# Optimization experiments

Hardware: AMD Instinct MI355X
Metric: run time of the kernel (lower is better)

## Reference

```python
import jax, jax.numpy as jnp
import numpy as np

D_MODEL = 2048
NUM_HEADS = 16
HEAD_DIM = D_MODEL // NUM_HEADS
SCALE = HEAD_DIM ** -0.5
ALPHA = 1.0


def setup_inputs() -> dict:
    key = jax.random.key(0)
    ks = jax.random.split(key, 9)
    B, T = 2, 2048
    s = 0.02
    w = lambda k: jax.random.normal(k, (D_MODEL, D_MODEL), jnp.float32) * s
    b = lambda k: jax.random.normal(k, (D_MODEL,), jnp.float32) * s
    return {
        'x': jax.random.normal(ks[0], (B, T, D_MODEL), jnp.float32),
        'q_w': w(ks[1]), 'q_b': b(ks[2]),
        'k_w': w(ks[3]), 'k_b': b(ks[4]),
        'v_w': w(ks[5]), 'v_b': b(ks[6]),
        'o_w': w(ks[7]), 'o_b': b(ks[8]),
    }


def reference(x, q_w, q_b, k_w, k_b, v_w, v_b, o_w, o_b):
    B, T, D = x.shape
    H, HD = NUM_HEADS, HEAD_DIM

    def proj_split(w, bias):
        y = x @ w.T + bias  # torch Linear: x @ W^T + b
        # B T (H D) -> (B H) T D
        return y.reshape(B, T, H, HD).transpose(0, 2, 1, 3).reshape(B * H, T, HD)

    Q = proj_split(q_w, q_b)
    K = proj_split(k_w, k_b)
    V = proj_split(v_w, v_b)

    # Note: original computes S[h,i,j] = K_i . Q_j (K first, Q second)
    S = jnp.einsum('hid,hjd->hij', K, Q) * SCALE  # (B*H, T, T)

    idx = jnp.arange(T)
    delta = idx[:, None] - idx[None, :]  # delta[i,j] = i - j
    # similarity_power_law decay: -(delta**alpha) for delta>=0, else 0
    decay = jnp.where(delta < 0, 0.0, -(delta.astype(jnp.float32) ** ALPHA))
    # causal mask: positions with j > i (delta < 0) set to -inf, then add decay
    S = jnp.where(delta < 0, -jnp.inf, S) + decay

    C = jax.nn.softmax(S, axis=-1)
    attn = jnp.einsum('hij,hjd->hid', C, V)  # (B*H, T, HD)
    # (B H) T D -> B T (H D)
    attn = attn.reshape(B, H, T, HD).transpose(0, 2, 1, 3).reshape(B, T, D)
    return attn @ o_w.T + o_b
```

## Files before the change

### kernel.cpp

```cpp
#include <hip/hip_runtime.h>
#include <hip/hip_bf16.h>
#include <stdint.h>

#define BT    4096
#define DM    2048
#define TSEQ  2048
#define NHEAD 16
#define HD    128
#define QKV_LD 6144
#define ATT_SCALE 0.088388347648318447f
#define WIN   64

typedef __attribute__((ext_vector_type(8))) short short8;
typedef __attribute__((ext_vector_type(4))) float f32x4;

__device__ __forceinline__ uint16_t f2bf(float f) {
  uint32_t u = __float_as_uint(f);
  return (uint16_t)((u + 0x7FFFu + ((u >> 16) & 1u)) >> 16);
}

__device__ __forceinline__ void gload_lds16(const void* g, void* l) {
  __builtin_amdgcn_global_load_lds((__attribute__((address_space(1))) void*)g,
                                   (__attribute__((address_space(3))) void*)l,
                                   16, 0, 0);
}

__global__ __launch_bounds__(256) void prep(const float* __restrict__ x,
                                            const float* __restrict__ qw,
                                            const float* __restrict__ kw,
                                            const float* __restrict__ vw,
                                            const float* __restrict__ ow,
                                            const float* __restrict__ qb,
                                            const float* __restrict__ kb,
                                            const float* __restrict__ vb,
                                            uint16_t* __restrict__ xb,
                                            uint16_t* __restrict__ wqkv,
                                            uint16_t* __restrict__ wo,
                                            float* __restrict__ bcat) {
  const int NX = BT * DM / 4;
  const int NW = DM * DM / 4;
  const int total = NX + 4 * NW;
  int i0 = blockIdx.x * 256 + threadIdx.x;
  for (int idx = i0; idx < total; idx += gridDim.x * 256) {
    const float* src;
    uint16_t* dst;
    int off;
    if (idx < NX)            { src = x;  dst = xb;                          off = idx; }
    else if (idx < NX + NW)  { src = qw; dst = wqkv;                        off = idx - NX; }
    else if (idx < NX + 2*NW){ src = kw; dst = wqkv + (size_t)DM * DM;      off = idx - NX - NW; }
    else if (idx < NX + 3*NW){ src = vw; dst = wqkv + (size_t)2 * DM * DM;  off = idx - NX - 2*NW; }
    else                     { src = ow; dst = wo;                          off = idx - NX - 3*NW; }
    float4 v = ((const float4*)src)[off];
    ushort4 o;
    o.x = f2bf(v.x); o.y = f2bf(v.y); o.z = f2bf(v.z); o.w = f2bf(v.w);
    ((ushort4*)dst)[off] = o;
  }
  if (i0 < 3 * DM) {
    float v = (i0 < DM) ? qb[i0] : (i0 < 2 * DM ? kb[i0 - DM] : vb[i0 - 2 * DM]);
    bcat[i0] = v;
  }
}

template <int MF, bool OUT_BF16>
__global__ __launch_bounds__(512, 1) void gemm_p4(const uint16_t* __restrict__ A,
                                                  const uint16_t* __restrict__ B,
                                                  const float* __restrict__ bias,
                                                  void* __restrict__ Cout,
                                                  int M, int N, int K) {
  constexpr int BM   = MF * 32;
  constexpr int ABUF = BM * 32;
  constexpr int BUFE = ABUF + 8192;
  constexpr int MB   = (MF == 8) ? 2 : 4;
  constexpr int NB   = 8 / MB;
  __shared__ uint16_t sm[4 * BUFE];

  const int tid = threadIdx.x;
  const int l   = tid & 63;
  const int wid = tid >> 6;
  const int wr  = wid >> 2;
  const int wc  = wid & 3;
  const int ln  = l & 15;
  const int g   = l >> 4;

  const int nbx    = N >> 8;
  const int bid    = blockIdx.x;
  const int xcd    = bid & 7;
  const int idx    = bid >> 3;
  const int rect_n = nbx / NB;
  const int rect_m = (M / BM) / MB;
  const int m_t    = (xcd / NB) * rect_m + idx / rect_n;
  const int n_t    = (xcd % NB) * rect_n + idx % rect_n;
  const int m0     = m_t * BM;
  const int n0     = n_t << 8;

  const int srow = l >> 2;
  const int gch  = (l & 3) ^ ((l >> 3) & 3);
  const uint16_t* pa  = A + (size_t)(m0 + wid * 16 + srow) * K + gch * 8;
  const uint16_t* pb0 = B + (size_t)(n0 + wid * 16 + srow) * K + gch * 8;
  const uint16_t* pb1 = B + (size_t)(n0 + 128 + wid * 16 + srow) * K + gch * 8;
  const int ldsA  = wid * 512;
  const int ldsB0 = ABUF + wid * 512;
  const int ldsB1 = ABUF + 4096 + wid * 512;

  const int pc = g ^ ((ln >> 1) & 3);

  f32x4 acc[MF][4];
#pragma unroll
  for (int i = 0; i < MF; ++i)
#pragma unroll
    for (int j = 0; j < 4; ++j) acc[i][j] = (f32x4){0.f, 0.f, 0.f, 0.f};

  const int nt = K >> 5;

#define STAGE(T)                                                        \
  {                                                                     \
    uint16_t* base_ = sm + (size_t)((T) & 3) * BUFE;                    \
    const size_t ko_ = (size_t)(T) * 32;                                \
    gload_lds16(pa + ko_, base_ + ldsA);                                \
    if (MF == 8) gload_lds16(pa + (size_t)128 * K + ko_, base_ + 4096 + ldsA); \
    gload_lds16(pb0 + ko_, base_ + ldsB0);                              \
    gload_lds16(pb1 + ko_, base_ + ldsB1);                              \
  }

#define COMPUTE(T)                                                      \
  {                                                                     \
    const uint16_t* buf_ = sm + (size_t)((T) & 3) * BUFE;               \
    short8 af_[MF], bf_[4];                                             \
    _Pragma("unroll")                                                   \
    for (int fi = 0; fi < MF; ++fi)                                     \
      af_[fi] = *(const short8*)(buf_ + (wr * (MF * 16) + fi * 16 + ln) * 32 + pc * 8); \
    _Pragma("unroll")                                                   \
    for (int fj = 0; fj < 4; ++fj)                                      \
      bf_[fj] = *(const short8*)(buf_ + ABUF + (wc * 64 + fj * 16 + ln) * 32 + pc * 8); \
    __builtin_amdgcn_s_setprio(1);                                      \
    _Pragma("unroll")                                                   \
    for (int fi = 0; fi < MF; ++fi)                                     \
      _Pragma("unroll")                                                 \
      for (int fj = 0; fj < 4; ++fj)                                    \
        acc[fi][fj] = __builtin_amdgcn_mfma_f32_16x16x32_bf16(          \
            af_[fi], bf_[fj], acc[fi][fj], 0, 0, 0);                    \
    __builtin_amdgcn_s_setprio(0);                                      \
  }

#define WAIT_LOOP()                                                     \
  if (MF == 8) asm volatile("s_waitcnt vmcnt(8)" ::: "memory");         \
  else         asm volatile("s_waitcnt vmcnt(6)" ::: "memory");
#define WAIT_PEEL1()                                                    \
  if (MF == 8) asm volatile("s_waitcnt vmcnt(4)" ::: "memory");         \
  else         asm volatile("s_waitcnt vmcnt(3)" ::: "memory");

  STAGE(0); STAGE(1); STAGE(2);
  WAIT_LOOP();
  __builtin_amdgcn_s_barrier();

#pragma unroll 1
  for (int t = 0; t < nt - 3; ++t) {
    STAGE(t + 3);
    COMPUTE(t);
    WAIT_LOOP();
    __builtin_amdgcn_s_barrier();
  }
  COMPUTE(nt - 3);
  WAIT_PEEL1();
  __builtin_amdgcn_s_barrier();
  COMPUTE(nt - 2);
  asm volatile("s_waitcnt vmcnt(0)" ::: "memory");
  __builtin_amdgcn_s_barrier();
  COMPUTE(nt - 1);
#undef STAGE
#undef COMPUTE
#undef WAIT_LOOP
#undef WAIT_PEEL1

  const int g4 = g * 4;
#pragma unroll
  for (int fi = 0; fi < MF; ++fi) {
    size_t row = (size_t)(m0 + wr * (MF * 16) + fi * 16 + g4);
#pragma unroll
    for (int fj = 0; fj < 4; ++fj) {
      int col = n0 + wc * 64 + fj * 16 + ln;
      float bv = bias[col];
#pragma unroll
      for (int r = 0; r < 4; ++r) {
        float v = acc[fi][fj][r] + bv;
        if (OUT_BF16) ((uint16_t*)Cout)[(row + r) * N + col] = f2bf(v);
        else          ((float*)Cout)[(row + r) * N + col] = v;
      }
    }
  }
}

__global__ __launch_bounds__(256) void attn_mfma(const uint16_t* __restrict__ QKV,
                                                 uint16_t* __restrict__ O) {
  __shared__ __align__(16) uint16_t smem[16384 + 17408];
  uint16_t* Qs = smem;
  uint16_t* Vt = smem + 16384;
  uint16_t* Pl = smem;

  const int tid  = threadIdx.x;
  const int lane = tid & 63;
  const int w    = tid >> 6;
  const int g    = lane >> 4;
  const int ln   = lane & 15;

  const int i0 = blockIdx.x * 64;
  const int h  = blockIdx.y;
  const int b  = blockIdx.z;
  const int wb = i0 - 63;
  const size_t hoff  = (size_t)h * HD;
  const size_t bbase = (size_t)b * TSEQ;

#pragma unroll
  for (int it = 0; it < 8; ++it) {
    int s   = it * 256 + tid;
    int row = s >> 4, c = s & 15;
    int j = wb + row;
    if (j >= 0 && j < TSEQ) {
      const uint16_t* gsrc = QKV + (bbase + j) * (size_t)QKV_LD + hoff
                           + (size_t)((c ^ (row & 7)) * 8);
      uint16_t* ldst = Qs + (size_t)(s & ~63) * 8;
      gload_lds16(gsrc, ldst);
    } else {
      uint4 z = {0, 0, 0, 0};
      *(uint4*)(Qs + (size_t)s * 8) = z;
    }
  }

#pragma unroll
  for (int it = 0; it < 4; ++it) {
    int s  = it * 256 + tid;
    int jp = (s & 15) | (it << 4);
    int dc = (s >> 4) & 15;
    int j0 = wb + 2 * jp;
    uint4 va = {0, 0, 0, 0}, vb = {0, 0, 0, 0};
    if (j0 >= 0 && j0 < TSEQ)
      va = *(const uint4*)(QKV + (bbase + j0) * (size_t)QKV_LD + 2 * DM + hoff + dc * 8);
    if (j0 + 1 >= 0 && j0 + 1 < TSEQ)
      vb = *(const uint4*)(QKV + (bbase + j0 + 1) * (size_t)QKV_LD + 2 * DM + hoff + dc * 8);
    const uint16_t* ap = (const uint16_t*)&va;
    const uint16_t* bp = (const uint16_t*)&vb;
#pragma unroll
    for (int t = 0; t < 8; ++t) {
      uint32_t pk = (uint32_t)ap[t] | ((uint32_t)bp[t] << 16);
      *(uint32_t*)(Vt + (size_t)(dc * 8 + t) * 136 + 2 * jp) = pk;
    }
  }

  short8 kreg[4];
  {
    const uint16_t* kp = QKV + (bbase + i0 + w * 16 + ln) * (size_t)QKV_LD
                       + DM + hoff + g * 8;
#pragma unroll
    for (int kc = 0; kc < 4; ++kc) kreg[kc] = *(const short8*)(kp + kc * 32);
  }

  __syncthreads();

  f32x4 acc[8];
#pragma unroll
  for (int nf = 0; nf < 8; ++nf) acc[nf] = (f32x4){0.f, 0.f, 0.f, 0.f};
#pragma unroll
  for (int kc = 0; kc < 4; ++kc) {
#pragma unroll
    for (int nf = 0; nf < 8; ++nf) {
      int row = nf * 16 + ln;
      int chunk = (kc * 4 + g) ^ (row & 7);
      short8 qf = *(const short8*)(Qs + (size_t)row * 128 + chunk * 8);
      acc[nf] = __builtin_amdgcn_mfma_f32_16x16x32_bf16(kreg[kc], qf, acc[nf], 0, 0, 0);
    }
  }

#pragma unroll
  for (int nf = 0; nf < 8; ++nf) {
    int rj = nf * 16 + ln;
    int jg = wb + rj;
#pragma unroll
    for (int r = 0; r < 4; ++r) {
      int il = w * 16 + g * 4 + r;
      int delta = il + 63 - rj;
      float v = acc[nf][r] * ATT_SCALE - (float)delta;
      acc[nf][r] = ((unsigned)delta < 64u && jg >= 0) ? v : -1e30f;
    }
  }

  float inv[4];
#pragma unroll
  for (int r = 0; r < 4; ++r) {
    float mx = acc[0][r];
#pragma unroll
    for (int nf = 1; nf < 8; ++nf) mx = fmaxf(mx, acc[nf][r]);
    mx = fmaxf(mx, __shfl_xor(mx, 1));
    mx = fmaxf(mx, __shfl_xor(mx, 2));
    mx = fmaxf(mx, __shfl_xor(mx, 4));
    mx = fmaxf(mx, __shfl_xor(mx, 8));
    float s = 0.f;
#pragma unroll
    for (int nf = 0; nf < 8; ++nf) {
      float e = __expf(acc[nf][r] - mx);
      acc[nf][r] = e;
      s += e;
    }
    s += __shfl_xor(s, 1);
    s += __shfl_xor(s, 2);
    s += __shfl_xor(s, 4);
    s += __shfl_xor(s, 8);
    inv[r] = 1.0f / s;
  }

  __syncthreads();

#pragma unroll
  for (int nf = 0; nf < 8; ++nf)
#pragma unroll
    for (int r = 0; r < 4; ++r)
      Pl[(size_t)(w * 16 + g * 4 + r) * 136 + nf * 16 + ln] = f2bf(acc[nf][r]);
  asm volatile("s_waitcnt lgkmcnt(0)" ::: "memory");
  __builtin_amdgcn_sched_barrier(0);

  f32x4 o[8];
#pragma unroll
  for (int nf = 0; nf < 8; ++nf) o[nf] = (f32x4){0.f, 0.f, 0.f, 0.f};
#pragma unroll
  for (int kc = 0; kc < 4; ++kc) {
    short8 pa = *(const short8*)(Pl + (size_t)(w * 16 + ln) * 136 + kc * 32 + g * 8);
#pragma unroll
    for (int nf = 0; nf < 8; ++nf) {
      short8 vbf = *(const short8*)(Vt + (size_t)(nf * 16 + ln) * 136 + kc * 32 + g * 8);
      o[nf] = __builtin_amdgcn_mfma_f32_16x16x32_bf16(pa, vbf, o[nf], 0, 0, 0);
    }
  }

  const size_t obase = (bbase + i0 + w * 16) * (size_t)DM + hoff;
#pragma unroll
  for (int nf = 0; nf < 8; ++nf)
#pragma unroll
    for (int r = 0; r < 4; ++r)
      O[obase + (size_t)(g * 4 + r) * DM + nf * 16 + ln] = f2bf(o[nf][r] * inv[r]);
}

extern "C" void kernel_launch(void* const* d_in, const int* in_sizes, int n_in,
                              void* d_out, int out_size, void* d_ws, size_t ws_size,
                              hipStream_t stream) {
  const float* x   = (const float*)d_in[0];
  const float* q_w = (const float*)d_in[1];
  const float* q_b = (const float*)d_in[2];
  const float* k_w = (const float*)d_in[3];
  const float* k_b = (const float*)d_in[4];
  const float* v_w = (const float*)d_in[5];
  const float* v_b = (const float*)d_in[6];
  const float* o_w = (const float*)d_in[7];
  const float* o_b = (const float*)d_in[8];

  char* ws = (char*)d_ws;
  const size_t XB_BYTES   = (size_t)BT * DM * 2;
  const size_t W_BYTES    = (size_t)DM * DM * 2;
  const size_t WQKV_BYTES = 3 * W_BYTES;

  uint16_t* xb   = (uint16_t*)(ws);
  uint16_t* wqkv = (uint16_t*)(ws + XB_BYTES);
  uint16_t* wo   = (uint16_t*)(ws + XB_BYTES + WQKV_BYTES);
  float*    bcat = (float*)   (ws + XB_BYTES + WQKV_BYTES + W_BYTES);
  uint16_t* QKVb = (uint16_t*)(ws + XB_BYTES + WQKV_BYTES + W_BYTES + 24576);

  prep<<<2048, 256, 0, stream>>>(x, q_w, k_w, v_w, o_w, q_b, k_b, v_b,
                                 xb, wqkv, wo, bcat);

  gemm_p4<8, true><<<(BT / 256) * (3 * DM / 256), 512, 0, stream>>>(
      xb, wqkv, bcat, QKVb, BT, 3 * DM, DM);

  dim3 ga(TSEQ / 64, NHEAD, 2);
  attn_mfma<<<ga, 256, 0, stream>>>(QKVb, xb);

  gemm_p4<4, false><<<(BT / 128) * (DM / 256), 512, 0, stream>>>(
      xb, wo, o_b, d_out, BT, DM, DM);
}
```

Baseline: 202.7 us.

## Add quarter-staged 256x256 GEMM with interleaved loads and MFMA for QKV projection

Adds a new QKV projection GEMM kernel that splits each 64-wide K tile into four half-tile stages. Each stage's global-to-LDS load is issued between fragment reads and MFMA groups, and raises wave priority around the MFMA bursts. It double-buffers LDS across K tiles, uses an XOR swizzle, and remaps blocks by XCD into rectangles to improve L2 locality. The aim is to hide memory latency better than the previous 4-buffer gemm_p4. It costs a full 128KB of LDS and relies on hand-tuned vmcnt waits, so correctness depends on the staging order.

Measured after the change: 191.3 us. 5.6% less time.

```diff
diff --git a/kernel.cpp b/kernel.cpp
--- a/kernel.cpp
+++ b/kernel.cpp
@@ -61,6 +61,176 @@
   }
 }
 
+template <bool OUT_BF16>
+__global__ __launch_bounds__(512, 1) void gemm8q(const uint16_t* __restrict__ A,
+                                                 const uint16_t* __restrict__ B,
+                                                 const float* __restrict__ bias,
+                                                 void* __restrict__ Cout,
+                                                 int M, int N, int K) {
+  __shared__ uint16_t sm[65536];
+
+  const int tid = threadIdx.x;
+  const int l   = tid & 63;
+  const int wid = tid >> 6;
+  const int wr  = wid >> 2;
+  const int wc  = wid & 3;
+  const int ln  = l & 15;
+  const int g   = l >> 4;
+
+  const int nbx    = N >> 8;
+  const int bid    = blockIdx.x;
+  const int xcd    = bid & 7;
+  const int idx    = bid >> 3;
+  const int rect_n = nbx >> 2;
+  const int rect_m = (M >> 8) >> 1;
+  const int m0     = ((xcd >> 2) * rect_m + idx / rect_n) << 8;
+  const int n0     = ((xcd & 3) * rect_n + idx % rect_n) << 8;
+
+  const int r0 = wid * 16 + (l >> 3);
+  const int c0 = (((l & 7) ^ (l >> 4)) << 3);
+  const int c1 = (((l & 7) ^ (l >> 4) ^ 4) << 3);
+  const uint16_t* gsA = A + (size_t)(m0 + r0) * K;
+  const uint16_t* gsB = B + (size_t)(n0 + r0) * K;
+
+  const int key  = (ln >> 1) & 7;
+  const int pc0  = ((g ^ key) << 3);
+  const int pc1  = (((4 + g) ^ key) << 3);
+  const int aoff = wr * 8192 + ln * 64;
+  const int boff = 16384 + (wc >> 1) * 8192 + ((wc & 1) * 64 + ln) * 64;
+
+  f32x4 acc[8][4];
+#pragma unroll
+  for (int i = 0; i < 8; ++i)
+#pragma unroll
+    for (int j = 0; j < 4; ++j) acc[i][j] = (f32x4){0.f, 0.f, 0.f, 0.f};
+
+  const int nt  = K >> 6;
+  const int nit = nt >> 1;
+
+#define STAGEH(T, H)                                                             \
+  if ((T) < nt) {                                                                \
+    const uint16_t* s_ = (((H) < 2) ? gsA : gsB) + (size_t)((H) & 1) * 128 * K   \
+                         + (size_t)(T) * 64;                                     \
+    uint16_t* d_ = sm + ((size_t)((T) & 1) * 32768 + (size_t)(H) * 8192 + wid * 1024); \
+    gload_lds16(s_ + c0, d_);                                                    \
+    gload_lds16(s_ + (size_t)8 * K + c1, d_ + 512);                             \
+  }
+
+#define FENCE() asm volatile("" ::: "memory")
+
+#define HALFIT(TC, S1T, S1H, S2T, S2H, S3T, S3H, S4T, S4H, LASTV)                \
+  {                                                                              \
+    const uint16_t* ab_ = sm + (size_t)((TC) & 1) * 32768 + aoff;                \
+    const uint16_t* bb_ = sm + (size_t)((TC) & 1) * 32768 + boff;                \
+    short8 af_[4][2], ag_[4][2], bf0_[2][2], bf1_[2][2];                         \
+          \
+    _Pragma("unroll")                                                            \
+    for (int mi = 0; mi < 4; ++mi) {                                             \
+      af_[mi][0] = *(const short8*)(ab_ + mi * 1024 + pc0);                      \
+      af_[mi][1] = *(const short8*)(ab_ + mi * 1024 + pc1);                      \
+    }                                                                            \
+    _Pragma("unroll")                                                            \
+    for (int nj = 0; nj < 2; ++nj) {                                             \
+      bf0_[nj][0] = *(const short8*)(bb_ + nj * 1024 + pc0);                     \
+      bf0_[nj][1] = *(const short8*)(bb_ + nj * 1024 + pc1);                     \
+    }                                                                            \
+    STAGEH(S1T, S1H);                                                            \
+    __builtin_amdgcn_s_setprio(1);                                               \
+    _Pragma("unroll")                                                            \
+    for (int kk = 0; kk < 2; ++kk)                                               \
+      _Pragma("unroll")                                                          \
+      for (int mi = 0; mi < 4; ++mi)                                             \
+        _Pragma("unroll")                                                        \
+        for (int nj = 0; nj < 2; ++nj)                                           \
+          acc[mi][nj] = __builtin_amdgcn_mfma_f32_16x16x32_bf16(                 \
+              af_[mi][kk], bf0_[nj][kk], acc[mi][nj], 0, 0, 0);                  \
+    __builtin_amdgcn_s_setprio(0);                                               \
+             \
+    _Pragma("unroll")                                                            \
+    for (int nj = 0; nj < 2; ++nj) {                                             \
+      bf1_[nj][0] = *(const short8*)(bb_ + (2 + nj) * 1024 + pc0);               \
+      bf1_[nj][1] = *(const short8*)(bb_ + (2 + nj) * 1024 + pc1);               \
+    }                                                                            \
+    STAGEH(S2T, S2H);                                                            \
+    __builtin_amdgcn_s_setprio(1);                                               \
+    _Pragma("unroll")                                                            \
+    for (int kk = 0; kk < 2; ++kk)                                               \
+      _Pragma("unroll")                                                          \
+      for (int mi = 0; mi < 4; ++mi)                                             \
+        _Pragma("unroll")                                                        \
+        for (int nj = 0; nj < 2; ++nj)                                           \
+          acc[mi][2 + nj] = __builtin_amdgcn_mfma_f32_16x16x32_bf16(             \
+              af_[mi][kk], bf1_[nj][kk], acc[mi][2 + nj], 0, 0, 0);              \
+    __builtin_amdgcn_s_setprio(0);                                               \
+    FENCE(); __builtin_amdgcn_s_barrier(); FENCE();           \
+           \
+    _Pragma("unroll")                                                            \
+    for (int mi = 0; mi < 4; ++mi) {                                             \
+      ag_[mi][0] = *(const short8*)(ab_ + (4 + mi) * 1024 + pc0);                \
+      ag_[mi][1] = *(const short8*)(ab_ + (4 + mi) * 1024 + pc1);                \
+    }                                                                            \
+    STAGEH(S3T, S3H);                                                            \
+    __builtin_amdgcn_s_setprio(1);                                               \
+    _Pragma("unroll")                                                            \
+    for (int kk = 0; kk < 2; ++kk)                                               \
+      _Pragma("unroll")                                                          \
+      for (int mi = 0; mi < 4; ++mi)                                             \
+        _Pragma("unroll")                                                        \
+        for (int nj = 0; nj < 2; ++nj)                                           \
+          acc[4 + mi][nj] = __builtin_amdgcn_mfma_f32_16x16x32_bf16(             \
+              ag_[mi][kk], bf0_[nj][kk], acc[4 + mi][nj], 0, 0, 0);              \
+    __builtin_amdgcn_s_setprio(0);                                               \
+               \
+    STAGEH(S4T, S4H);                                                            \
+    __builtin_amdgcn_s_setprio(1);                                               \
+    _Pragma("unroll")                                                            \
+    for (int kk = 0; kk < 2; ++kk)                                               \
+      _Pragma("unroll")                                                          \
+      for (int mi = 0; mi < 4; ++mi)                                             \
+        _Pragma("unroll")                                                        \
+        for (int nj = 0; nj < 2; ++nj)                                           \
+          acc[4 + mi][2 + nj] = __builtin_amdgcn_mfma_f32_16x16x32_bf16(         \
+              ag_[mi][kk], bf1_[nj][kk], acc[4 + mi][2 + nj], 0, 0, 0);          \
+    __builtin_amdgcn_s_setprio(0);                                               \
+    FENCE();                                                                     \
+    if (LASTV) asm volatile("s_waitcnt vmcnt(0)" ::: "memory");                  \
+    else       asm volatile("s_waitcnt vmcnt(4)" ::: "memory");                  \
+    __builtin_amdgcn_s_barrier(); FENCE();                                       \
+  }
+
+  STAGEH(0, 0); STAGEH(0, 1); STAGEH(0, 2); STAGEH(0, 3);
+  STAGEH(1, 2); STAGEH(1, 3);
+  asm volatile("s_waitcnt vmcnt(4)" ::: "memory");
+  FENCE(); __builtin_amdgcn_s_barrier(); FENCE();
+
+#pragma unroll 1
+  for (int i = 0; i < nit; ++i) {
+    const int t1 = 2 * i + 1, t2 = 2 * i + 2, t3 = 2 * i + 3;
+    HALFIT(2 * i, t1, 0, t1, 1, t2, 2, t2, 3, (i == nit - 1));
+    HALFIT(t1, t2, 0, t2, 1, t3, 2, t3, 3, 0);
+  }
+#undef HALFIT
+#undef STAGEH
+#undef FENCE
+
+  const int g4 = g * 4;
+#pragma unroll
+  for (int mi = 0; mi < 8; ++mi) {
+    size_t row = (size_t)(m0 + wr * 128 + mi * 16 + g4);
+#pragma unroll
+    for (int nj = 0; nj < 4; ++nj) {
+      int col = n0 + wc * 64 + nj * 16 + ln;
+      float bv = bias[col];
+#pragma unroll
+      for (int r = 0; r < 4; ++r) {
+        float v = acc[mi][nj][r] + bv;
+        if (OUT_BF16) ((uint16_t*)Cout)[(row + r) * N + col] = f2bf(v);
+        else          ((float*)Cout)[(row + r) * N + col] = v;
+      }
+    }
+  }
+}
+
 template <int MF, bool OUT_BF16>
 __global__ __launch_bounds__(512, 1) void gemm_p4(const uint16_t* __restrict__ A,
                                                   const uint16_t* __restrict__ B,
@@ -365,7 +535,7 @@
   prep<<<2048, 256, 0, stream>>>(x, q_w, k_w, v_w, o_w, q_b, k_b, v_b,
                                  xb, wqkv, wo, bcat);
 
-  gemm_p4<8, true><<<(BT / 256) * (3 * DM / 256), 512, 0, stream>>>(
+  gemm8q<true><<<(BT / 256) * (3 * DM / 256), 512, 0, stream>>>(
       xb, wqkv, bcat, QKVb, BT, 3 * DM, DM);
 
   dim3 ga(TSEQ / 64, NHEAD, 2);
```

## Add 256x384-tile QKV GEMM kernel sized to launch exactly one wave

Applied to the files above, without the earlier changes.

Replaces the generic 256x256-tile QKV projection GEMM with a dedicated kernel that uses 256x384 output tiles, so the grid is 256 blocks instead of 384. The aim is to avoid the partial second wave and to raise per-block reuse of the A tiles. It uses XCD-aware block-to-tile mapping, double-buffered direct-to-LDS loads and interleaved MFMA phases. The larger accumulator footprint raises register pressure and lengthens the epilogue.

Result: faster. 173.3 us (-14.5%).

```diff
diff --git a/kernel.cpp b/kernel.cpp
--- a/kernel.cpp
+++ b/kernel.cpp
@@ -61,6 +61,123 @@
   }
 }
 
+__global__ __launch_bounds__(512, 1) void gemm384(const uint16_t* __restrict__ A,
+                                                  const uint16_t* __restrict__ B,
+                                                  const float* __restrict__ bias,
+                                                  uint16_t* __restrict__ Cout) {
+  __shared__ uint16_t sm[81920];
+
+  const int tid = threadIdx.x;
+  const int l   = tid & 63;
+  const int wid = tid >> 6;
+  const int wr  = wid >> 2;
+  const int wc  = wid & 3;
+  const int ln  = l & 15;
+  const int g   = l >> 4;
+
+  const int bid = blockIdx.x;
+  const int xcd = bid & 7;
+  const int idx = bid >> 3;
+  const int m0  = ((xcd >> 2) * 8 + (idx >> 2)) << 8;
+  const int n0  = ((xcd & 3) * 4 + (idx & 3)) * 384;
+
+  const int s_r = wid * 8 + (l >> 3);
+  const int s_c = ((l & 7) ^ ((wid * 4 + (l >> 4)) & 7)) << 3;
+  const uint16_t* gA = A + (size_t)(m0 + s_r) * DM + s_c;
+  const uint16_t* gB = B + (size_t)(n0 + s_r) * DM + s_c;
+  const int sdst = wid * 512;
+
+  const int key  = (ln >> 1) & 7;
+  const int pc0  = (g ^ key) << 3;
+  const int pc1  = ((4 + g) ^ key) << 3;
+  const int aoff = (wr * 128 + ln) * 64;
+  const int boff = 16384 + (wc * 96 + ln) * 64;
+
+  f32x4 acc[8][6];
+#pragma unroll
+  for (int i = 0; i < 8; ++i)
+#pragma unroll
+    for (int j = 0; j < 6; ++j) acc[i][j] = (f32x4){0.f, 0.f, 0.f, 0.f};
+
+  const int nt = DM >> 6;
+
+#define STA(T, U)                                                                \
+  if ((T) < nt) {                                                                \
+    const uint16_t* s_ = gA + (size_t)((U) * 128) * DM + (size_t)(T) * 64;       \
+    uint16_t* d_ = sm + ((T) & 1) * 40960 + (U) * 8192 + sdst;                   \
+    gload_lds16(s_, d_);                                                         \
+    gload_lds16(s_ + (size_t)64 * DM, d_ + 4096);                                \
+  }
+#define STB(T, U)                                                                \
+  if ((T) < nt) {                                                                \
+    const uint16_t* s_ = gB + (size_t)((U) * 128) * DM + (size_t)(T) * 64;       \
+    uint16_t* d_ = sm + ((T) & 1) * 40960 + 16384 + (U) * 8192 + sdst;           \
+    gload_lds16(s_, d_);                                                         \
+    gload_lds16(s_ + (size_t)64 * DM, d_ + 4096);                                \
+  }
+#define FENCE() asm volatile("" ::: "memory")
+
+#define MMH(BUFP, MH, PC)                                                        \
+  __builtin_amdgcn_s_setprio(1);                                                 \
+  _Pragma("unroll")                                                              \
+  for (int mi = 0; mi < 4; ++mi) {                                               \
+    short8 af = *(const short8*)((BUFP) + aoff + ((MH) * 64 + mi * 16) * 64 + (PC)); \
+    _Pragma("unroll")                                                            \
+    for (int nj = 0; nj < 6; ++nj)                                               \
+      acc[(MH) * 4 + mi][nj] = __builtin_amdgcn_mfma_f32_16x16x32_bf16(          \
+          af, bf[nj], acc[(MH) * 4 + mi][nj], 0, 0, 0);                          \
+  }                                                                              \
+  __builtin_amdgcn_s_setprio(0);
+
+  STA(0, 0); STA(0, 1);
+  STB(0, 0); STB(0, 1); STB(0, 2);
+  STB(1, 0); STB(1, 1); STB(1, 2);
+  asm volatile("s_waitcnt vmcnt(6)" ::: "memory");
+  FENCE(); __builtin_amdgcn_s_barrier(); FENCE();
+
+#pragma unroll 1
+  for (int t = 0; t < nt; ++t) {
+    const uint16_t* bufp = sm + (size_t)(t & 1) * 40960;
+    short8 bf[6];
+#pragma unroll
+    for (int nj = 0; nj < 6; ++nj)
+      bf[nj] = *(const short8*)(bufp + boff + nj * 1024 + pc0);
+    STA(t + 1, 0);
+    MMH(bufp, 0, pc0);
+    STA(t + 1, 1);
+    MMH(bufp, 1, pc0);
+#pragma unroll
+    for (int nj = 0; nj < 6; ++nj)
+      bf[nj] = *(const short8*)(bufp + boff + nj * 1024 + pc1);
+    MMH(bufp, 0, pc1);
+    FENCE(); __builtin_amdgcn_s_barrier(); FENCE();
+    STB(t + 2, 0); STB(t + 2, 1); STB(t + 2, 2);
+    MMH(bufp, 1, pc1);
+    FENCE();
+    if (t < nt - 2)       asm volatile("s_waitcnt vmcnt(6)" ::: "memory");
+    else if (t == nt - 2) asm volatile("s_waitcnt vmcnt(0)" ::: "memory");
+    __builtin_amdgcn_s_barrier(); FENCE();
+  }
+#undef MMH
+#undef STA
+#undef STB
+#undef FENCE
+
+  const int g4 = g * 4;
+#pragma unroll
+  for (int a = 0; a < 8; ++a) {
+    size_t row = (size_t)(m0 + wr * 128 + (a >> 2) * 64 + (a & 3) * 16 + g4);
+#pragma unroll
+    for (int nj = 0; nj < 6; ++nj) {
+      int col = n0 + wc * 96 + nj * 16 + ln;
+      float bv = bias[col];
+#pragma unroll
+      for (int r = 0; r < 4; ++r)
+        Cout[(row + r) * QKV_LD + col] = f2bf(acc[a][nj][r] + bv);
+    }
+  }
+}
+
 template <int MF, bool OUT_BF16>
 __global__ __launch_bounds__(512, 1) void gemm_p4(const uint16_t* __restrict__ A,
                                                   const uint16_t* __restrict__ B,
@@ -365,8 +482,7 @@
   prep<<<2048, 256, 0, stream>>>(x, q_w, k_w, v_w, o_w, q_b, k_b, v_b,
                                  xb, wqkv, wo, bcat);
 
-  gemm_p4<8, true><<<(BT / 256) * (3 * DM / 256), 512, 0, stream>>>(
-      xb, wqkv, bcat, QKVb, BT, 3 * DM, DM);
+  gemm384<<<256, 512, 0, stream>>>(xb, wqkv, bcat, QKVb);
 
   dim3 ga(TSEQ / 64, NHEAD, 2);
   attn_mfma<<<ga, 256, 0, stream>>>(QKVb, xb);
```
